# Optimization experiments

Hardware: AMD Instinct MI355X
Metric: run time of the kernel (lower is better)

## Reference

```python
import jax, jax.numpy as jnp
import numpy as np


def setup_inputs() -> dict:
    key = jax.random.key(0)
    k = jax.random.split(key, 6)
    N, Cin, H, W = 16, 256, 14, 14   # ROI mask features
    D = 256                          # dim_reduced
    C = 20                           # number of FALKON classifiers (num_classes - 1)
    M = 512                          # max Nystrom centers (padded)
    x = jax.random.normal(k[0], (N, Cin, H, W), jnp.float32)
    # torch ConvTranspose2d weight layout: [in, out, kH, kW]
    conv_w = jax.random.normal(k[1], (Cin, D, 2, 2), jnp.float32) * 0.05
    conv_b = jnp.zeros((D,), jnp.float32)
    mean = jax.random.normal(k[2], (D,), jnp.float32) * 0.1
    mean_norm = jnp.full((1,), 10.0, jnp.float32)
    ny = jax.random.normal(k[3], (C, M, D), jnp.float32)
    alpha = jax.random.normal(k[4], (C, M, 1), jnp.float32) * 0.01
    sigma = jnp.full((1,), 25.0, jnp.float32)
    return {"x": x, "conv_w": conv_w, "conv_b": conv_b, "mean": mean,
            "mean_norm": mean_norm, "ny": ny, "alpha": alpha, "sigma": sigma}


def reference(x, conv_w, conv_b, mean, mean_norm, ny, alpha, sigma):
    N, Cin, H, W = x.shape
    D = conv_w.shape[1]
    C = ny.shape[0]
    # ConvTranspose2d(kernel=2, stride=2, pad=0): each input pixel expands to a 2x2 block.
    y = jnp.einsum('nchw,coij->nohiwj', x, conv_w).reshape(N, D, 2 * H, 2 * W)
    y = jax.nn.relu(y + conv_b[None, :, None, None])
    fw = y.shape[2]                                   # feat_width = 28
    # permute(0,2,3,1).reshape(-1, D): pixel order (roi, h, w)
    f = y.transpose(0, 2, 3, 1).reshape(-1, D)        # [P, D], P = N*fw*fw
    f = (f - mean) * (20.0 / mean_norm[0])
    # Batched Gaussian kernel mmv: K[c,p,m] = exp(-||f_p - ny_cm||^2 / (2 sigma^2))
    sq = (jnp.sum(f * f, axis=-1)[None, :, None]
          + jnp.sum(ny * ny, axis=-1)[:, None, :]
          - 2.0 * jnp.einsum('pd,cmd->cpm', f, ny))   # [C, P, M]
    K = jnp.exp(-sq / (2.0 * sigma[0] ** 2))
    scores = jnp.einsum('cpm,cm->cp', K, alpha[..., 0])  # [C, P]
    P = f.shape[0]
    bg = jnp.full((P, 1), -2.0, f.dtype)              # background column of -2
    ps = jnp.concatenate([bg, scores.T], axis=1)      # [P, C+1]
    # per-ROI: [fw*fw, C+1].T.reshape(C+1, fw, fw) == reshape(N, fw, fw, C+1) -> NCHW
    out = ps.reshape(N, fw, fw, C + 1).transpose(0, 3, 1, 2)
    return out
```

## Files before the change

### kernel.cpp

```cpp
#include <hip/hip_runtime.h>

typedef __bf16 bf16_t;
typedef __bf16 bf16x8 __attribute__((ext_vector_type(8)));
typedef __bf16 bf16x4 __attribute__((ext_vector_type(4)));
typedef float  f32x4  __attribute__((ext_vector_type(4)));
typedef float  f32x16 __attribute__((ext_vector_type(16)));
typedef char   i8x16  __attribute__((ext_vector_type(16)));
typedef char   i8x4   __attribute__((ext_vector_type(4)));
typedef int    i32x4  __attribute__((ext_vector_type(4)));

#define PIX 196
#define P_  12544
#define M_  512
#define SF  12.0f
#define SN  24.0f

__device__ inline void gload_lds16(const void* g, void* l) {
  __builtin_amdgcn_global_load_lds((const __attribute__((address_space(1))) void*)g,
                                   (__attribute__((address_space(3))) void*)l,
                                   16, 0, 0);
}

__global__ __launch_bounds__(256) void k_wtb(const float* __restrict__ conv_w,
                                             bf16_t* __restrict__ wtb) {
  int c = blockIdx.x, d = threadIdx.x;
  f32x4 w = *reinterpret_cast<const f32x4*>(conv_w + (c * 256 + d) * 4);
  int ks = c >> 4, kb = (c >> 3) & 1, j = c & 7;
#pragma unroll
  for (int q = 0; q < 4; ++q) {
    int col = q * 256 + d;
    int cf = col >> 5;
    int lfrag = kb * 32 + (col & 31);
    wtb[((cf * 16 + ks) * 64 + lfrag) * 8 + j] = (bf16_t)w[q];
  }
}

__global__ __launch_bounds__(256) void k_xt(const float* __restrict__ x,
                                            bf16_t* __restrict__ xb) {
  __shared__ float xs[64][198];
  int n = blockIdx.x, c0 = blockIdx.y * 64;
  int t = threadIdx.x;
  const float* xp = x + (n * 256 + c0) * PIX;
#pragma unroll 7
  for (int r = 0; r < 49; ++r) {
    int idx = r * 256 + t;
    xs[idx / PIX][idx % PIX] = xp[idx];
  }
  __syncthreads();
  for (int r = 0; r < 13; ++r) {
    int idx = r * 256 + t;
    if (idx < 3136) {
      int hw = idx >> 4, c4 = idx & 15;
      bf16x4 h;
#pragma unroll
      for (int i = 0; i < 4; ++i) h[i] = (bf16_t)xs[c4 * 4 + i][hw];
      *reinterpret_cast<bf16x4*>(xb + (n * PIX + hw) * 256 + c0 + c4 * 4) = h;
    }
  }
}

__global__ __launch_bounds__(256) void k_nyprep(const float* __restrict__ ny,
                                                const float* __restrict__ alpha,
                                                const float* __restrict__ sigma,
                                                char* __restrict__ nys8,
                                                float* __restrict__ e_n) {
  int l = threadIdx.x & 63;
  int row = blockIdx.x * 4 + (threadIdx.x >> 6);
  int c = row >> 9, m = row & 511;
  f32x4 v = *reinterpret_cast<const f32x4*>(ny + row * 256 + l * 4);
  i8x4 q8;
  float sq = 0.f;
#pragma unroll
  for (int i = 0; i < 4; ++i) {
    float fq = fminf(fmaxf(__builtin_rintf(v[i] * SN), -127.f), 127.f);
    q8[i] = (char)(int)fq;
    float fv = fq * (1.f / SN);
    sq += fv * fv;
  }
  int u = m >> 5, mf = (m >> 4) & 1, mc = m & 15;
  int ks = l >> 4, lg = (l >> 2) & 3, j0 = (l & 3) * 4;
  *reinterpret_cast<i8x4*>(nys8 + (c * 16 + u) * 8192 + mf * 4096 + ks * 1024 +
                           (lg * 16 + mc) * 16 + j0) = q8;
#pragma unroll
  for (int o = 1; o < 64; o <<= 1) sq += __shfl_xor(sq, o);
  if (l == 0) {
    float s = sigma[0];
    e_n[row] = __expf(-sq / (2.f * s * s)) * alpha[row];
  }
}

__global__ __launch_bounds__(256) void k_convT(const bf16_t* __restrict__ xb,
                                               const bf16_t* __restrict__ wtb,
                                               const float* __restrict__ conv_b,
                                               const float* __restrict__ mean,
                                               const float* __restrict__ mean_norm,
                                               char* __restrict__ fb8) {
  __shared__ bf16_t bs[32768];
  int rb = blockIdx.x * 64, cbase = blockIdx.y * 128;
  int tid = threadIdx.x, w = tid >> 6, l = tid & 63;
  int wr = w >> 1, wc = w & 1;
  const bf16_t* bsrc = wtb + blockIdx.y * 32768;
#pragma unroll
  for (int r = 0; r < 16; ++r) {
    int s = (r * 4 + w) * 64 + l;
    gload_lds16(bsrc + s * 8, bs + s * 8);
  }
  bf16x8 a[16];
  {
    const bf16_t* ap = xb + (rb + wr * 32 + (l & 31)) * 256 + (l >> 5) * 8;
#pragma unroll
    for (int ks = 0; ks < 16; ++ks) a[ks] = *reinterpret_cast<const bf16x8*>(ap + ks * 16);
  }
  __syncthreads();
  float scale = (20.f / mean_norm[0]) * SF;
  int hi = l >> 5;
#pragma unroll
  for (int cf = 0; cf < 2; ++cf) {
    f32x16 acc = {0.f,0.f,0.f,0.f,0.f,0.f,0.f,0.f,0.f,0.f,0.f,0.f,0.f,0.f,0.f,0.f};
#pragma unroll
    for (int ks = 0; ks < 16; ++ks) {
      bf16x8 b = *reinterpret_cast<const bf16x8*>(bs + ((wc * 2 + cf) * 16 + ks) * 512 + l * 8);
      acc = __builtin_amdgcn_mfma_f32_32x32x16_bf16(a[ks], b, acc, 0, 0, 0);
    }
    int col = cbase + wc * 64 + cf * 32 + (l & 31);
    int q = col >> 8, d = col & 255;
    float bias = conv_b[d], mn = mean[d];
    int qi = q >> 1, qj = q & 1;
#pragma unroll
    for (int r = 0; r < 16; ++r) {
      int p3 = rb + wr * 32 + (r & 3) + 8 * (r >> 2) + 4 * hi;
      int n = p3 / PIX, hw = p3 % PIX;
      int h = hw / 14, ww = hw % 14;
      int p = n * 784 + (2 * h + qi) * 28 + 2 * ww + qj;
      float v = fmaxf(acc[r] + bias, 0.f);
      float fq = fminf(fmaxf(__builtin_rintf((v - mn) * scale), -127.f), 127.f);
      fb8[p * 256 + d] = (char)(int)fq;
    }
  }
}

__global__ __launch_bounds__(256, 3) void k_falkon(const char* __restrict__ fb8,
                                                   const char* __restrict__ nys8,
                                                   const float* __restrict__ e_n,
                                                   const float* __restrict__ sigma,
                                                   float* __restrict__ out) {
  __shared__ char bs[2][8192];
  __shared__ float lds_en[512];
  int c = blockIdx.y, pb = blockIdx.x * 128;
  int tid = threadIdx.x, w = tid >> 6, l = tid & 63;

  if (c == 0 && tid < 128) {
    int p = pb + tid;
    out[(p / 784) * 16464 + (p % 784)] = -2.0f;
  }

  lds_en[tid] = e_n[c * M_ + tid];
  lds_en[256 + tid] = e_n[c * M_ + 256 + tid];

  i32x4 a[2][4];
  {
    const char* ap = fb8 + (pb + w * 32 + (l & 15)) * 256 + (l >> 4) * 16;
#pragma unroll
    for (int rf = 0; rf < 2; ++rf)
#pragma unroll
      for (int ks = 0; ks < 4; ++ks)
        a[rf][ks] = *reinterpret_cast<const i32x4*>(ap + rf * 16 * 256 + ks * 64);
  }

  float sg = sigma[0];
  float kl = 1.44269504088896340736f / (sg * sg);
  float Ksc = kl * (1.f / (SF * SN));

  float ef0, ef1;
#pragma unroll
  for (int rf = 0; rf < 2; ++rf) {
    int ssi = 0;
#pragma unroll
    for (int ks = 0; ks < 4; ++ks) {
      i8x16 q = __builtin_bit_cast(i8x16, a[rf][ks]);
#pragma unroll
      for (int j = 0; j < 16; ++j) {
        int qv = (signed char)q[j];
        ssi += qv * qv;
      }
    }
    ssi += __shfl_xor(ssi, 16);
    ssi += __shfl_xor(ssi, 32);
    float ef = __builtin_amdgcn_exp2f(-(float)ssi * (0.5f * kl / (SF * SF)));
    if (rf == 0) ef0 = ef; else ef1 = ef;
  }

  f32x4 sacc[2];
  sacc[0] = {0.f, 0.f, 0.f, 0.f};
  sacc[1] = {0.f, 0.f, 0.f, 0.f};

  const char* nb = nys8 + c * (16 * 8192);

  auto stage = [&](int u) {
    const char* src = nb + u * 8192;
    char* dst = &bs[u & 1][0];
#pragma unroll
    for (int r = 0; r < 2; ++r) {
      int slot = r * 256 + tid;
      gload_lds16(src + slot * 16, dst + slot * 16);
    }
  };

  stage(0);
  stage(1);
  asm volatile("s_waitcnt vmcnt(2) lgkmcnt(0)" ::: "memory");
  __builtin_amdgcn_s_barrier();

  for (int u = 0; u < 16; ++u) {
    const char* bp = &bs[u & 1][0] + l * 16;
    i32x4 b[2][4];
#pragma unroll
    for (int mf = 0; mf < 2; ++mf)
#pragma unroll
      for (int ks = 0; ks < 4; ++ks)
        b[mf][ks] = *reinterpret_cast<const i32x4*>(bp + mf * 4096 + ks * 1024);

    i32x4 acc[2][2];
#pragma unroll
    for (int rf = 0; rf < 2; ++rf)
#pragma unroll
      for (int mf = 0; mf < 2; ++mf) acc[rf][mf] = {0, 0, 0, 0};

    __builtin_amdgcn_s_setprio(1);
#pragma unroll
    for (int ks = 0; ks < 4; ++ks)
#pragma unroll
      for (int rf = 0; rf < 2; ++rf)
#pragma unroll
        for (int mf = 0; mf < 2; ++mf)
          acc[rf][mf] = __builtin_amdgcn_mfma_i32_16x16x64_i8(a[rf][ks], b[mf][ks],
                                                              acc[rf][mf], 0, 0, 0);
    __builtin_amdgcn_s_setprio(0);

    float en0 = lds_en[u * 32 + (l & 15)];
    float en1 = lds_en[u * 32 + 16 + (l & 15)];
#pragma unroll
    for (int rf = 0; rf < 2; ++rf)
#pragma unroll
      for (int r = 0; r < 4; ++r) {
        sacc[rf][r] += en0 * __builtin_amdgcn_exp2f((float)acc[rf][0][r] * Ksc)
                     + en1 * __builtin_amdgcn_exp2f((float)acc[rf][1][r] * Ksc);
      }

    if (u < 15) {
      asm volatile("s_waitcnt lgkmcnt(0)" ::: "memory");
      __builtin_amdgcn_s_barrier();
      if (u + 2 < 16) {
        stage(u + 2);
        asm volatile("s_waitcnt vmcnt(2)" ::: "memory");
      } else {
        asm volatile("s_waitcnt vmcnt(0)" ::: "memory");
      }
      __builtin_amdgcn_s_barrier();
    }
  }

#pragma unroll
  for (int rf = 0; rf < 2; ++rf)
#pragma unroll
    for (int r = 0; r < 4; ++r) {
      float v = sacc[rf][r];
      v += __shfl_xor(v, 1);
      v += __shfl_xor(v, 2);
      v += __shfl_xor(v, 4);
      v += __shfl_xor(v, 8);
      int rr = (l >> 4) * 4 + r;
      float ef = __shfl(rf == 0 ? ef0 : ef1, rr);
      if ((l & 15) == 0) {
        int p = pb + w * 32 + rf * 16 + rr;
        out[(p / 784) * 16464 + (c + 1) * 784 + (p % 784)] = v * ef;
      }
    }
}

extern "C" void kernel_launch(void* const* d_in, const int* in_sizes, int n_in,
                              void* d_out, int out_size, void* d_ws, size_t ws_size,
                              hipStream_t stream) {
  const float* x         = (const float*)d_in[0];
  const float* conv_w    = (const float*)d_in[1];
  const float* conv_b    = (const float*)d_in[2];
  const float* mean      = (const float*)d_in[3];
  const float* mean_norm = (const float*)d_in[4];
  const float* ny        = (const float*)d_in[5];
  const float* alpha     = (const float*)d_in[6];
  const float* sigma     = (const float*)d_in[7];
  float* out = (float*)d_out;

  char* ws = (char*)d_ws;
  bf16_t* wtb  = (bf16_t*)ws;
  bf16_t* xb   = (bf16_t*)(ws + 524288);
  char*   fb8  = (char*)(ws + 2129920);
  char*   nys8 = (char*)(ws + 5341184);
  float*  e_n  = (float*)(ws + 7962624);

  k_wtb<<<dim3(256), dim3(256), 0, stream>>>(conv_w, wtb);
  k_xt<<<dim3(16, 4), dim3(256), 0, stream>>>(x, xb);
  k_nyprep<<<dim3(2560), dim3(256), 0, stream>>>(ny, alpha, sigma, nys8, e_n);
  k_convT<<<dim3(49, 8), dim3(256), 0, stream>>>(xb, wtb, conv_b, mean, mean_norm, fb8);
  k_falkon<<<dim3(98, 20), dim3(256), 0, stream>>>(fb8, nys8, e_n, sigma, out);
}
```

Before: 75.26 us.

## Merge three prep kernels into one launch and raise falkon occupancy bound

```diff
diff --git a/kernel.cpp b/kernel.cpp
--- a/kernel.cpp
+++ b/kernel.cpp
@@ -21,71 +21,73 @@
                                    16, 0, 0);
 }
 
-__global__ __launch_bounds__(256) void k_wtb(const float* __restrict__ conv_w,
-                                             bf16_t* __restrict__ wtb) {
-  int c = blockIdx.x, d = threadIdx.x;
-  f32x4 w = *reinterpret_cast<const f32x4*>(conv_w + (c * 256 + d) * 4);
-  int ks = c >> 4, kb = (c >> 3) & 1, j = c & 7;
-#pragma unroll
-  for (int q = 0; q < 4; ++q) {
-    int col = q * 256 + d;
-    int cf = col >> 5;
-    int lfrag = kb * 32 + (col & 31);
-    wtb[((cf * 16 + ks) * 64 + lfrag) * 8 + j] = (bf16_t)w[q];
-  }
-}
-
-__global__ __launch_bounds__(256) void k_xt(const float* __restrict__ x,
-                                            bf16_t* __restrict__ xb) {
-  __shared__ float xs[64][198];
-  int n = blockIdx.x, c0 = blockIdx.y * 64;
-  int t = threadIdx.x;
-  const float* xp = x + (n * 256 + c0) * PIX;
-#pragma unroll 7
-  for (int r = 0; r < 49; ++r) {
-    int idx = r * 256 + t;
-    xs[idx / PIX][idx % PIX] = xp[idx];
-  }
-  __syncthreads();
-  for (int r = 0; r < 13; ++r) {
-    int idx = r * 256 + t;
-    if (idx < 3136) {
-      int hw = idx >> 4, c4 = idx & 15;
-      bf16x4 h;
-#pragma unroll
-      for (int i = 0; i < 4; ++i) h[i] = (bf16_t)xs[c4 * 4 + i][hw];
-      *reinterpret_cast<bf16x4*>(xb + (n * PIX + hw) * 256 + c0 + c4 * 4) = h;
-    }
-  }
-}
-
-__global__ __launch_bounds__(256) void k_nyprep(const float* __restrict__ ny,
-                                                const float* __restrict__ alpha,
-                                                const float* __restrict__ sigma,
-                                                char* __restrict__ nys8,
-                                                float* __restrict__ e_n) {
-  int l = threadIdx.x & 63;
-  int row = blockIdx.x * 4 + (threadIdx.x >> 6);
-  int c = row >> 9, m = row & 511;
-  f32x4 v = *reinterpret_cast<const f32x4*>(ny + row * 256 + l * 4);
-  i8x4 q8;
-  float sq = 0.f;
-#pragma unroll
-  for (int i = 0; i < 4; ++i) {
-    float fq = fminf(fmaxf(__builtin_rintf(v[i] * SN), -127.f), 127.f);
-    q8[i] = (char)(int)fq;
-    float fv = fq * (1.f / SN);
-    sq += fv * fv;
-  }
-  int u = m >> 5, mf = (m >> 4) & 1, mc = m & 15;
-  int ks = l >> 4, lg = (l >> 2) & 3, j0 = (l & 3) * 4;
-  *reinterpret_cast<i8x4*>(nys8 + (c * 16 + u) * 8192 + mf * 4096 + ks * 1024 +
-                           (lg * 16 + mc) * 16 + j0) = q8;
-#pragma unroll
-  for (int o = 1; o < 64; o <<= 1) sq += __shfl_xor(sq, o);
-  if (l == 0) {
-    float s = sigma[0];
-    e_n[row] = __expf(-sq / (2.f * s * s)) * alpha[row];
+__global__ __launch_bounds__(256) void k_prep(const float* __restrict__ conv_w,
+                                              const float* __restrict__ x,
+                                              const float* __restrict__ ny,
+                                              const float* __restrict__ alpha,
+                                              const float* __restrict__ sigma,
+                                              bf16_t* __restrict__ wtb,
+                                              bf16_t* __restrict__ xb,
+                                              char* __restrict__ nys8,
+                                              float* __restrict__ e_n) {
+  __shared__ float xs[16][198];
+  int bid = blockIdx.x, tid = threadIdx.x;
+  if (bid < 2560) {
+    int l = tid & 63;
+    int row = bid * 4 + (tid >> 6);
+    int c = row >> 9, m = row & 511;
+    f32x4 v = *reinterpret_cast<const f32x4*>(ny + row * 256 + l * 4);
+    i8x4 q8;
+    float sq = 0.f;
+#pragma unroll
+    for (int i = 0; i < 4; ++i) {
+      float fq = fminf(fmaxf(__builtin_rintf(v[i] * SN), -127.f), 127.f);
+      q8[i] = (char)(int)fq;
+      float fv = fq * (1.f / SN);
+      sq += fv * fv;
+    }
+    int u = m >> 5, mf = (m >> 4) & 1, mc = m & 15;
+    int ks = l >> 4, lg = (l >> 2) & 3, j0 = (l & 3) * 4;
+    *reinterpret_cast<i8x4*>(nys8 + (c * 16 + u) * 8192 + mf * 4096 + ks * 1024 +
+                             (lg * 16 + mc) * 16 + j0) = q8;
+#pragma unroll
+    for (int o = 1; o < 64; o <<= 1) sq += __shfl_xor(sq, o);
+    if (l == 0) {
+      float s = sigma[0];
+      e_n[row] = __expf(-sq / (2.f * s * s)) * alpha[row];
+    }
+  } else if (bid < 2816) {
+    int c = bid - 2560, d = tid;
+    f32x4 w = *reinterpret_cast<const f32x4*>(conv_w + (c * 256 + d) * 4);
+    int ks = c >> 4, kb = (c >> 3) & 1, j = c & 7;
+#pragma unroll
+    for (int q = 0; q < 4; ++q) {
+      int col = q * 256 + d;
+      int cf = col >> 5;
+      int lfrag = kb * 32 + (col & 31);
+      wtb[((cf * 16 + ks) * 64 + lfrag) * 8 + j] = (bf16_t)w[q];
+    }
+  } else {
+    int idx2 = bid - 2816;
+    int n = idx2 >> 4, c0 = (idx2 & 15) * 16;
+    const float* xp = x + (n * 256 + c0) * PIX;
+#pragma unroll
+    for (int r = 0; r < 13; ++r) {
+      int idx = r * 256 + tid;
+      if (idx < 3136) xs[idx / PIX][idx % PIX] = xp[idx];
+    }
+    __syncthreads();
+#pragma unroll
+    for (int r = 0; r < 4; ++r) {
+      int idx = r * 256 + tid;
+      if (idx < 784) {
+        int hw = idx >> 2, c4 = idx & 3;
+        bf16x4 h;
+#pragma unroll
+        for (int i = 0; i < 4; ++i) h[i] = (bf16_t)xs[c4 * 4 + i][hw];
+        *reinterpret_cast<bf16x4*>(xb + (n * PIX + hw) * 256 + c0 + c4 * 4) = h;
+      }
+    }
   }
 }
 
@@ -139,7 +141,7 @@
   }
 }
 
-__global__ __launch_bounds__(256, 3) void k_falkon(const char* __restrict__ fb8,
+__global__ __launch_bounds__(256, 7) void k_falkon(const char* __restrict__ fb8,
                                                    const char* __restrict__ nys8,
                                                    const float* __restrict__ e_n,
                                                    const float* __restrict__ sigma,
@@ -298,9 +300,8 @@
   char*   nys8 = (char*)(ws + 5341184);
   float*  e_n  = (float*)(ws + 7962624);
 
-  k_wtb<<<dim3(256), dim3(256), 0, stream>>>(conv_w, wtb);
-  k_xt<<<dim3(16, 4), dim3(256), 0, stream>>>(x, xb);
-  k_nyprep<<<dim3(2560), dim3(256), 0, stream>>>(ny, alpha, sigma, nys8, e_n);
+  k_prep<<<dim3(3072), dim3(256), 0, stream>>>(conv_w, x, ny, alpha, sigma,
+                                               wtb, xb, nys8, e_n);
   k_convT<<<dim3(49, 8), dim3(256), 0, stream>>>(xb, wtb, conv_b, mean, mean_norm, fb8);
   k_falkon<<<dim3(98, 20), dim3(256), 0, stream>>>(fb8, nys8, e_n, sigma, out);
 }
```

Result: slower. 182.5 us (+142.4%).
